# Kernel optimization log

Measured on AMD Instinct MI355X. Metric: run time of the kernel, lower is better.

The kernel has to match this reference:

```python
import jax, jax.numpy as jnp
import numpy as np

B, T, C, H = 256, 256, 512, 64  # batch, seq, n_embd, head_size


def setup_inputs() -> dict:
    key = jax.random.key(0)
    kx, kk, kq, kv = jax.random.split(key, 4)
    x = jax.random.normal(kx, (B, T, C), dtype=jnp.float32)
    # nn.Linear(C, H, bias=False): store as [C, H] so y = x @ W
    Wk = jax.random.normal(kk, (C, H), dtype=jnp.float32) * (C ** -0.5)
    Wq = jax.random.normal(kq, (C, H), dtype=jnp.float32) * (C ** -0.5)
    Wv = jax.random.normal(kv, (C, H), dtype=jnp.float32) * (C ** -0.5)
    return {"x": x, "Wk": Wk, "Wq": Wq, "Wv": Wv}


def reference(x, Wk, Wq, Wv):
    Bx, Tx, Cx = x.shape
    k = jnp.einsum('btc,ch->bth', x, Wk)
    q = jnp.einsum('btc,ch->bth', x, Wq)
    v = jnp.einsum('btc,ch->bth', x, Wv)
    # NOTE: original scales by C**-0.5 (embed dim), not head_size**-0.5
    wei = jnp.einsum('bth,bsh->bts', q, k) * (Cx ** -0.5)  # [B,T,T]
    causal = jnp.tril(jnp.ones((Tx, Tx), dtype=bool))
    wei = jnp.where(causal, wei, -jnp.inf)
    wei = jax.nn.softmax(wei, axis=-1)
    # dropout is identity at inference (deterministic reference)
    out = jnp.einsum('bts,bsh->bth', wei, v)  # [B,T,H]
    return out
```

## Files before the change

### kernel.cpp

```cpp
#include <hip/hip_runtime.h>

#define BB 256
#define TT 256
#define CC 512
#define HH 64

typedef __bf16 bf16;
typedef __bf16 bf16x4 __attribute__((ext_vector_type(4)));
typedef __bf16 bf16x8 __attribute__((ext_vector_type(8)));
typedef float  f32x4  __attribute__((ext_vector_type(4)));

#define MFMA16(a, b, c) __builtin_amdgcn_mfma_f32_16x16x32_bf16((a), (b), (c), 0, 0, 0)

typedef __attribute__((address_space(1))) const void cas1_void;
typedef __attribute__((address_space(3))) void as3_void;
__device__ __forceinline__ void g2lds16(const void* g, void* l) {
    __builtin_amdgcn_global_load_lds((cas1_void*)g, (as3_void*)l, 16, 0, 0);
}

__global__ __launch_bounds__(256) void wtrans(const float* __restrict__ Wk,
                                              const float* __restrict__ Wq,
                                              const float* __restrict__ Wv,
                                              bf16* __restrict__ wt) {
    int which = blockIdx.y;
    const float* W = (which == 0) ? Wq : (which == 1) ? Wk : Wv;
    int idx = blockIdx.x * 256 + threadIdx.x;
    int n = idx & 63, k4 = idx >> 6;
    bf16x4 o;
    #pragma unroll
    for (int i = 0; i < 4; ++i) o[i] = (bf16)W[(k4 * 4 + i) * HH + n];
    *(bf16x4*)(&wt[which * (CC * HH) + n * CC + k4 * 4]) = o;
}

__global__ __launch_bounds__(256, 2) void qkv_gemm(const float* __restrict__ x,
                                                   const bf16* __restrict__ wt,
                                                   bf16* __restrict__ q,
                                                   bf16* __restrict__ k,
                                                   bf16* __restrict__ vt) {
    __shared__ float xs[128 * 64];
    __shared__ bf16  wts[192 * 64];
    const int tid  = threadIdx.x;
    const int wv   = tid >> 6;
    const int lane = tid & 63;
    const int quad = lane >> 4;
    const int l15  = lane & 15;
    const int l7   = l15 & 7;
    const int rows0 = blockIdx.x * 128;

    f32x4 acc[2][12];
    #pragma unroll
    for (int mt = 0; mt < 2; ++mt)
        #pragma unroll
        for (int nt = 0; nt < 12; ++nt)
            acc[mt][nt] = (f32x4){0.f, 0.f, 0.f, 0.f};

    for (int kc = 0; kc < 8; ++kc) {
        __syncthreads();
        #pragma unroll
        for (int j = 0; j < 8; ++j) {
            int s = j * 256 + tid;
            int r = s >> 4, up = s & 15;
            int u = up ^ (r & 15);
            const float* gp = x + (size_t)(rows0 + r) * CC + kc * 64 + u * 4;
            g2lds16(gp, (char*)xs + (j * 256 + wv * 64) * 16);
        }
        #pragma unroll
        for (int j = 0; j < 6; ++j) {
            int n0 = wv * 48 + j * 8;
            int n  = n0 + (lane >> 3);
            int u  = (lane & 7) ^ (n & 7);
            const bf16* gp = wt + (size_t)n * CC + kc * 64 + u * 8;
            g2lds16(gp, (char*)wts + n0 * 128);
        }
        __syncthreads();

        #pragma unroll
        for (int mt = 0; mt < 2; ++mt) {
            int row = wv * 32 + mt * 16 + l15;
            const char* rp = (const char*)xs + row * 256;
            f32x4 x0 = *(const f32x4*)(rp + (((quad * 2)     ^ l15) * 16));
            f32x4 x1 = *(const f32x4*)(rp + (((quad * 2 + 1) ^ l15) * 16));
            f32x4 x2 = *(const f32x4*)(rp + (((8 + quad * 2)     ^ l15) * 16));
            f32x4 x3 = *(const f32x4*)(rp + (((8 + quad * 2 + 1) ^ l15) * 16));
            bf16x8 a0, a1;
            #pragma unroll
            for (int j = 0; j < 4; ++j) {
                a0[j] = (bf16)x0[j]; a0[j + 4] = (bf16)x1[j];
                a1[j] = (bf16)x2[j]; a1[j + 4] = (bf16)x3[j];
            }
            #pragma unroll
            for (int nt = 0; nt < 12; ++nt) {
                int n = (nt >> 2) * 64 + (nt & 3) * 16 + l15;
                const char* np = (const char*)wts + n * 128;
                bf16x8 b0 = *(const bf16x8*)(np + ((quad ^ l7) * 16));
                bf16x8 b1 = *(const bf16x8*)(np + (((4 + quad) ^ l7) * 16));
                acc[mt][nt] = MFMA16(a0, b0, acc[mt][nt]);
                acc[mt][nt] = MFMA16(a1, b1, acc[mt][nt]);
            }
        }
    }

    const float scale = 0.044194173824159216f;
    #pragma unroll
    for (int mt = 0; mt < 2; ++mt) {
        int gt = rows0 + wv * 32 + mt * 16 + quad * 4;
        #pragma unroll
        for (int nt = 0; nt < 12; ++nt) {
            int h = (nt & 3) * 16 + l15;
            int wch = nt >> 2;
            if (wch == 0) {
                #pragma unroll
                for (int r = 0; r < 4; ++r)
                    q[(gt + r) * HH + h] = (bf16)(acc[mt][nt][r] * scale);
            } else if (wch == 1) {
                #pragma unroll
                for (int r = 0; r < 4; ++r)
                    k[(gt + r) * HH + h] = (bf16)(acc[mt][nt][r]);
            } else {
                int bb = gt >> 8;
                int tloc = gt & 255;
                bf16x4 pv;
                #pragma unroll
                for (int r = 0; r < 4; ++r) pv[r] = (bf16)(acc[mt][nt][r]);
                *(bf16x4*)(&vt[(bb * HH + h) * TT + tloc]) = pv;
            }
        }
    }
}

__global__ __launch_bounds__(512) void attn(const bf16* __restrict__ q,
                                            const bf16* __restrict__ k,
                                            const bf16* __restrict__ vt,
                                            float* __restrict__ out) {
    __shared__ bf16 ks[256 * 64];
    __shared__ bf16 vs[64 * 256];
    __shared__ bf16 pbuf[8][16 * 264];
    const int tid  = threadIdx.x;
    const int wv   = tid >> 6;
    const int lane = tid & 63;
    const int quad = lane >> 4;
    const int l15  = lane & 15;
    const int b    = blockIdx.x;

    #pragma unroll
    for (int j = 0; j < 4; ++j) {
        int c = wv * 4 + j;
        int s = c * 64 + lane;
        {
            int r = s >> 3, up = s & 7, u = up ^ (r & 7);
            const bf16* gk = k + ((size_t)b * TT + r) * HH + u * 8;
            g2lds16(gk, (char*)ks + c * 1024);
        }
        {
            int r = s >> 5, up = s & 31, u = up ^ (r & 31);
            const bf16* gv = vt + ((size_t)b * HH + r) * TT + u * 8;
            g2lds16(gv, (char*)vs + c * 1024);
        }
    }
    __syncthreads();

    bf16* pb = &pbuf[wv][0];
    const int l7 = l15 & 7;

    #pragma unroll
    for (int ti = 0; ti < 2; ++ti) {
        const int rt = (ti == 0) ? wv : (15 - wv);
        const int rowbase = rt * 16;
        const int ctmax = rt;

        const bf16* qrow = q + ((size_t)b * TT + rowbase + l15) * HH;
        bf16x8 bq0 = *(const bf16x8*)(qrow + quad * 8);
        bf16x8 bq1 = *(const bf16x8*)(qrow + 32 + quad * 8);

        f32x4 sv[16];
        #pragma unroll
        for (int ct = 0; ct < 16; ++ct) {
            if (ct <= ctmax) {
                const char* kp = (const char*)ks + (ct * 16 + l15) * 128;
                bf16x8 k0 = *(const bf16x8*)(kp + ((quad ^ l7) * 16));
                bf16x8 k1 = *(const bf16x8*)(kp + (((4 + quad) ^ l7) * 16));
                f32x4 a = (f32x4){0.f, 0.f, 0.f, 0.f};
                a = MFMA16(k0, bq0, a);
                a = MFMA16(k1, bq1, a);
                int t = rowbase + l15;
                #pragma unroll
                for (int r = 0; r < 4; ++r) {
                    int s = ct * 16 + quad * 4 + r;
                    sv[ct][r] = (s <= t) ? a[r] : -3.0e38f;
                }
            }
        }

        float mx = -3.0e38f;
        #pragma unroll
        for (int ct = 0; ct < 16; ++ct)
            if (ct <= ctmax) {
                #pragma unroll
                for (int r = 0; r < 4; ++r) mx = fmaxf(mx, sv[ct][r]);
            }
        mx = fmaxf(mx, __shfl_xor(mx, 16));
        mx = fmaxf(mx, __shfl_xor(mx, 32));

        float sm = 0.f;
        #pragma unroll
        for (int ct = 0; ct < 16; ++ct) {
            if (ct <= ctmax) {
                bf16x4 ev;
                #pragma unroll
                for (int r = 0; r < 4; ++r) {
                    float e = __expf(sv[ct][r] - mx);
                    sm += e;
                    ev[r] = (bf16)e;
                }
                *(bf16x4*)(&pb[l15 * 264 + ct * 16 + quad * 4]) = ev;
            }
        }
        if (!(ctmax & 1)) {
            int ctz = ctmax + 1;
            *(bf16x4*)(&pb[l15 * 264 + ctz * 16 + quad * 4]) =
                (bf16x4){(bf16)0.f, (bf16)0.f, (bf16)0.f, (bf16)0.f};
        }
        sm += __shfl_xor(sm, 16);
        sm += __shfl_xor(sm, 32);
        asm volatile("" ::: "memory");

        f32x4 o[4];
        #pragma unroll
        for (int ht = 0; ht < 4; ++ht) o[ht] = (f32x4){0.f, 0.f, 0.f, 0.f};
        #pragma unroll
        for (int ks2 = 0; ks2 < 8; ++ks2) {
            if (ks2 <= (ctmax >> 1)) {
                bf16x8 pf = *(const bf16x8*)(&pb[l15 * 264 + ks2 * 32 + quad * 8]);
                #pragma unroll
                for (int ht = 0; ht < 4; ++ht) {
                    int vr = ht * 16 + l15;
                    bf16x8 vf = *(const bf16x8*)((const char*)vs + vr * 512
                                                 + (((ks2 * 4 + quad) ^ (vr & 31)) * 16));
                    o[ht] = MFMA16(vf, pf, o[ht]);
                }
            }
        }

        float rinv = 1.0f / sm;
        int t = rowbase + l15;
        #pragma unroll
        for (int ht = 0; ht < 4; ++ht) {
            f32x4 ov;
            #pragma unroll
            for (int r = 0; r < 4; ++r) ov[r] = o[ht][r] * rinv;
            *(f32x4*)(&out[((size_t)b * TT + t) * HH + ht * 16 + quad * 4]) = ov;
        }
        asm volatile("" ::: "memory");
    }
}

extern "C" void kernel_launch(void* const* d_in, const int* in_sizes, int n_in,
                              void* d_out, int out_size, void* d_ws, size_t ws_size,
                              hipStream_t stream) {
    const float* x  = (const float*)d_in[0];
    const float* Wk = (const float*)d_in[1];
    const float* Wq = (const float*)d_in[2];
    const float* Wv = (const float*)d_in[3];

    bf16* ws = (bf16*)d_ws;
    bf16* wt = ws;
    bf16* q  = ws + 3 * CC * HH;
    bf16* k  = q + (size_t)BB * TT * HH;
    bf16* vt = k + (size_t)BB * TT * HH;
    float* out = (float*)d_out;

    wtrans<<<dim3(32, 3), 256, 0, stream>>>(Wk, Wq, Wv, wt);
    qkv_gemm<<<dim3(512), 256, 0, stream>>>(x, wt, q, k, vt);
    attn<<<dim3(256), 512, 0, stream>>>(q, k, vt, out);
}
```

Measured before the change: 216.2 us.

## Double-buffer QKV GEMM LDS tiles with half-size K chunks

The QKV projection GEMM now uses two LDS buffers, each holding a 32-wide K chunk, instead of one 64-wide buffer. The async global-to-LDS loads for the next chunk are issued before computing on the current one, and the swizzle patterns are adjusted to the narrower rows. The aim is to overlap global memory latency with MFMA work and to remove one barrier per iteration. In exchange there are twice as many loop iterations and smaller per-iteration MFMA batches, while total LDS use stays the same.

Result: no change. 214.8 us (-0.7%).

```diff
diff --git a/kernel.cpp b/kernel.cpp
--- a/kernel.cpp
+++ b/kernel.cpp
@@ -37,15 +37,35 @@
                                                    bf16* __restrict__ q,
                                                    bf16* __restrict__ k,
                                                    bf16* __restrict__ vt) {
-    __shared__ float xs[128 * 64];
-    __shared__ bf16  wts[192 * 64];
+    __shared__ float xs[2][128 * 32];
+    __shared__ bf16  wts[2][192 * 32];
     const int tid  = threadIdx.x;
     const int wv   = tid >> 6;
     const int lane = tid & 63;
     const int quad = lane >> 4;
     const int l15  = lane & 15;
     const int l7   = l15 & 7;
+    const int l3   = l15 & 3;
     const int rows0 = blockIdx.x * 128;
+
+    auto stage = [&](int p, int kc) {
+        #pragma unroll
+        for (int j = 0; j < 4; ++j) {
+            int s = j * 256 + tid;
+            int r = s >> 3, up = s & 7;
+            int u = up ^ (r & 7);
+            const float* gp = x + (size_t)(rows0 + r) * CC + kc * 32 + u * 4;
+            g2lds16(gp, (char*)&xs[p][0] + (j * 256 + wv * 64) * 16);
+        }
+        #pragma unroll
+        for (int j = 0; j < 3; ++j) {
+            int n0 = wv * 48 + j * 16;
+            int n  = n0 + (lane >> 2);
+            int u  = (lane & 3) ^ (n & 3);
+            const bf16* gp = wt + (size_t)n * CC + kc * 32 + u * 8;
+            g2lds16(gp, (char*)&wts[p][0] + n0 * 64);
+        }
+    };
 
     f32x4 acc[2][12];
     #pragma unroll
@@ -54,50 +74,35 @@
         for (int nt = 0; nt < 12; ++nt)
             acc[mt][nt] = (f32x4){0.f, 0.f, 0.f, 0.f};
 
-    for (int kc = 0; kc < 8; ++kc) {
-        __syncthreads();
-        #pragma unroll
-        for (int j = 0; j < 8; ++j) {
-            int s = j * 256 + tid;
-            int r = s >> 4, up = s & 15;
-            int u = up ^ (r & 15);
-            const float* gp = x + (size_t)(rows0 + r) * CC + kc * 64 + u * 4;
-            g2lds16(gp, (char*)xs + (j * 256 + wv * 64) * 16);
-        }
-        #pragma unroll
-        for (int j = 0; j < 6; ++j) {
-            int n0 = wv * 48 + j * 8;
-            int n  = n0 + (lane >> 3);
-            int u  = (lane & 7) ^ (n & 7);
-            const bf16* gp = wt + (size_t)n * CC + kc * 64 + u * 8;
-            g2lds16(gp, (char*)wts + n0 * 128);
-        }
-        __syncthreads();
-
+    stage(0, 0);
+    __syncthreads();
+
+    for (int kc = 0; kc < 16; ++kc) {
+        int p = kc & 1;
+        if (kc < 15) stage(p ^ 1, kc + 1);
+
+        const char* xbase = (const char*)&xs[p][0];
+        const char* wbase = (const char*)&wts[p][0];
         #pragma unroll
         for (int mt = 0; mt < 2; ++mt) {
             int row = wv * 32 + mt * 16 + l15;
-            const char* rp = (const char*)xs + row * 256;
-            f32x4 x0 = *(const f32x4*)(rp + (((quad * 2)     ^ l15) * 16));
-            f32x4 x1 = *(const f32x4*)(rp + (((quad * 2 + 1) ^ l15) * 16));
-            f32x4 x2 = *(const f32x4*)(rp + (((8 + quad * 2)     ^ l15) * 16));
-            f32x4 x3 = *(const f32x4*)(rp + (((8 + quad * 2 + 1) ^ l15) * 16));
-            bf16x8 a0, a1;
+            const char* rp = xbase + row * 128;
+            f32x4 x0 = *(const f32x4*)(rp + (((quad * 2)     ^ l7) * 16));
+            f32x4 x1 = *(const f32x4*)(rp + (((quad * 2 + 1) ^ l7) * 16));
+            bf16x8 a0;
             #pragma unroll
             for (int j = 0; j < 4; ++j) {
                 a0[j] = (bf16)x0[j]; a0[j + 4] = (bf16)x1[j];
-                a1[j] = (bf16)x2[j]; a1[j + 4] = (bf16)x3[j];
             }
             #pragma unroll
             for (int nt = 0; nt < 12; ++nt) {
                 int n = (nt >> 2) * 64 + (nt & 3) * 16 + l15;
-                const char* np = (const char*)wts + n * 128;
-                bf16x8 b0 = *(const bf16x8*)(np + ((quad ^ l7) * 16));
-                bf16x8 b1 = *(const bf16x8*)(np + (((4 + quad) ^ l7) * 16));
+                const char* np = wbase + n * 64;
+                bf16x8 b0 = *(const bf16x8*)(np + ((quad ^ l3) * 16));
                 acc[mt][nt] = MFMA16(a0, b0, acc[mt][nt]);
-                acc[mt][nt] = MFMA16(a1, b1, acc[mt][nt]);
-            }
-        }
+            }
+        }
+        if (kc < 15) __syncthreads();
     }
 
     const float scale = 0.044194173824159216f;
```
